# Optimization experiments

Hardware: AMD Instinct MI355X
Metric: run time of the kernel (lower is better)

## Reference

```python
import jax, jax.numpy as jnp
import numpy as np

V = 1_000_000   # number of nodes in graph (embedding table rows)
D_IN = 128      # input feature dim
D_OUT = 384     # output dim (3 * D_OUT//3)
N_UNIQ = 20_000 # unique nodes in batch
K = 32          # neighbors per node (num_walks)
B = 40_000      # batch of node lookups


def setup_inputs() -> dict:
    key = jax.random.key(0)
    ks = jax.random.split(key, 12)
    d3 = D_OUT // 3
    return {
        "unique_nodes": jax.random.randint(ks[0], (N_UNIQ,), 0, V),
        "adj_neighbors": jax.random.randint(ks[1], (N_UNIQ, K), 0, V),
        "dis_neighbors": jax.random.randint(ks[2], (N_UNIQ, K), 0, V),
        "nodes_idx": jax.random.randint(ks[3], (B,), 0, N_UNIQ),
        "feat_table": jax.random.normal(ks[4], (V, D_IN), dtype=jnp.float32),
        # linear weights stored [in, out] (transposed vs torch nn.Linear)
        "W_self": jax.random.uniform(ks[5], (D_IN, d3), minval=-0.1, maxval=0.1, dtype=jnp.float32),
        "W_adj": jax.random.uniform(ks[6], (D_IN, d3), minval=-0.1, maxval=0.1, dtype=jnp.float32),
        "W_dis": jax.random.uniform(ks[7], (D_IN, d3), minval=-0.1, maxval=0.1, dtype=jnp.float32),
        "bias": jnp.zeros((D_OUT,), dtype=jnp.float32),
        "WC_w": jax.random.normal(ks[8], (D_OUT, D_OUT), dtype=jnp.float32) * 0.05,
        "WC_b": jnp.zeros((D_OUT,), dtype=jnp.float32),
    }


def reference(unique_nodes, adj_neighbors, dis_neighbors, nodes_idx,
              feat_table, W_self, W_adj, W_dis, bias, WC_w, WC_b):
    # MeanAggregator: one-hot mask.mm(embed) == mean of gathered neighbor feats
    adj_agg = jnp.mean(feat_table[adj_neighbors], axis=1)   # [N,K,D] -> [N,D]
    dis_agg = jnp.mean(feat_table[dis_neighbors], axis=1)
    self_feats = feat_table[unique_nodes] @ W_self           # [N, D_OUT/3]
    adj_feats = adj_agg @ W_adj
    dis_feats = dis_agg @ W_dis
    # concat + bias, WC linear, leakyReLU(0.2), L2-normalize (eval mode: no dropout)
    feats = jnp.concatenate([self_feats, adj_feats, dis_feats], axis=-1) + bias
    feats = feats @ WC_w + WC_b
    feats = jnp.where(feats >= 0, feats, 0.2 * feats)
    norm = jnp.maximum(jnp.linalg.norm(feats, axis=-1, keepdims=True), 1e-12)
    feats = feats / norm
    return feats[nodes_idx]  # [B, D_OUT]
```

## Files before the change

### kernel.cpp

```cpp
#include <hip/hip_runtime.h>
#include <hip/hip_bf16.h>

#define N_UNIQ 20000
#define K_NBR 32
#define BATCH 40000

typedef unsigned short ushort_t;
typedef __bf16 bfrag __attribute__((ext_vector_type(8)));
typedef float  ffrag __attribute__((ext_vector_type(4)));
typedef unsigned uvec4 __attribute__((ext_vector_type(4)));

__device__ __forceinline__ ushort_t f2bf(float f) {
    unsigned u = __builtin_bit_cast(unsigned, f);
    unsigned r = u + 0x7fffu + ((u >> 16) & 1u);
    return (ushort_t)(r >> 16);
}
__device__ __forceinline__ unsigned pack2(float x, float y) {
    return (unsigned)f2bf(x) | ((unsigned)f2bf(y) << 16);
}

__global__ void pack_agg_kernel(const float* __restrict__ Ws,
                                const float* __restrict__ Wa,
                                const float* __restrict__ Wd,
                                const float* __restrict__ WC,
                                uint4* __restrict__ wp1,
                                uint4* __restrict__ wp2,
                                const int* __restrict__ uniq,
                                const int* __restrict__ adjn,
                                const int* __restrict__ disn,
                                const float* __restrict__ feat,
                                ushort_t* __restrict__ F) {
    if (blockIdx.x < 96) {
        int t = blockIdx.x * blockDim.x + threadIdx.x;
        int l = t & 63, q = l >> 4, m = l & 15;
        ushort_t v[8];
        if (t < 6144) {
            int g   = t >> 11;
            int rem = t & 2047;
            int nt  = rem >> 8;
            int kk  = (rem >> 6) & 3;
            const float* W = (g == 0) ? Ws : ((g == 1) ? Wa : Wd);
#pragma unroll
            for (int j = 0; j < 8; j++)
                v[j] = f2bf(W[(kk * 32 + q * 8 + j) * 128 + nt * 16 + m]);
            uint4 u; __builtin_memcpy(&u, v, 16);
            wp1[t] = u;
        } else {
            int t2 = t - 6144;
            int nt = t2 / 768;
            int kk = (t2 >> 6) % 12;
#pragma unroll
            for (int j = 0; j < 8; j++)
                v[j] = f2bf(WC[(kk * 32 + q * 8 + j) * 384 + nt * 16 + m]);
            uint4 u; __builtin_memcpy(&u, v, 16);
            wp2[t2] = u;
        }
        return;
    }

    int node = ((blockIdx.x - 96) << 2) + (threadIdx.x >> 6);
    node = __builtin_amdgcn_readfirstlane(node);
    if (node >= N_UNIQ) return;

    const int l   = threadIdx.x & 63;
    const int lm  = l & 31;
    const bool isdis = (l >= 32);

    const int* __restrict__ na = adjn + node * K_NBR;
    const int* __restrict__ nd = disn + node * K_NBR;
    const float4* __restrict__ feat4 = (const float4*)feat;

    float ax = 0.f, ay = 0.f, az = 0.f, aw = 0.f;
#pragma unroll
    for (int i = 0; i < K_NBR; i++) {
        int ra = na[i];
        int rd = nd[i];
        int r  = isdis ? rd : ra;
        int idx = r * 32 + lm;
        float4 v = feat4[idx];
        ax += v.x; ay += v.y; az += v.z; aw += v.w;
    }

    const float inv = 1.0f / 32.0f;
    ushort_t* row = F + (size_t)node * 384;

    uint2 mpk;
    mpk.x = pack2(ax * inv, ay * inv);
    mpk.y = pack2(az * inv, aw * inv);
    *(uint2*)(row + 128 + (isdis ? 128 : 0) + lm * 4) = mpk;

    if (!isdis) {
        int rs = uniq[node];
        float4 sv = feat4[rs * 32 + lm];
        uint2 spk;
        spk.x = pack2(sv.x, sv.y);
        spk.y = pack2(sv.z, sv.w);
        *(uint2*)(row + lm * 4) = spk;
    }
}

__global__ void gemm1_kernel(ushort_t* __restrict__ F,
                             const uint4* __restrict__ wp1,
                             const float* __restrict__ bias) {
    int wv = blockIdx.x * 4 + (threadIdx.x >> 6);
    if (wv >= N_UNIQ / 16) return;
    int l = threadIdx.x & 63, q = l >> 4, m = l & 15;
    int m0 = wv * 16;

    uint4 a[12];
    const ushort_t* xrow = F + (size_t)(m0 + m) * 384;
#pragma unroll
    for (int kk = 0; kk < 12; kk++)
        a[kk] = *(const uint4*)(xrow + kk * 32 + q * 8);

    ushort_t outv[24][4];
#pragma unroll
    for (int nt = 0; nt < 24; nt++) {
        int g = nt >> 3;
        ffrag acc = {0.f, 0.f, 0.f, 0.f};
        const uint4* wp = wp1 + (size_t)nt * 4 * 64;
#pragma unroll
        for (int kk = 0; kk < 4; kk++) {
            bfrag bf = __builtin_bit_cast(bfrag, wp[kk * 64 + l]);
            bfrag af = __builtin_bit_cast(bfrag, a[g * 4 + kk]);
            acc = __builtin_amdgcn_mfma_f32_16x16x32_bf16(af, bf, acc, 0, 0, 0);
        }
        float bv = bias[nt * 16 + m];
#pragma unroll
        for (int r = 0; r < 4; r++) outv[nt][r] = f2bf(acc[r] + bv);
    }
#pragma unroll
    for (int nt = 0; nt < 24; nt++) {
        int col = nt * 16 + m;
#pragma unroll
        for (int r = 0; r < 4; r++)
            F[(size_t)(m0 + q * 4 + r) * 384 + col] = outv[nt][r];
    }
}

__global__ void gemm2_kernel(const ushort_t* __restrict__ F,
                             const uint4* __restrict__ wp2,
                             const float* __restrict__ wcb,
                             float* __restrict__ G) {
    int wv = blockIdx.x * 4 + (threadIdx.x >> 6);
    if (wv >= N_UNIQ / 16) return;
    int l = threadIdx.x & 63, q = l >> 4, m = l & 15;
    int m0 = wv * 16;

    uint4 a[12];
    const ushort_t* xrow = F + (size_t)(m0 + m) * 384;
#pragma unroll
    for (int kk = 0; kk < 12; kk++)
        a[kk] = *(const uint4*)(xrow + kk * 32 + q * 8);

    float vals[24][4];
    float ss[4] = {0.f, 0.f, 0.f, 0.f};
#pragma unroll
    for (int nt = 0; nt < 24; nt++) {
        ffrag acc = {0.f, 0.f, 0.f, 0.f};
        const uint4* wp = wp2 + (size_t)nt * 12 * 64;
#pragma unroll
        for (int kk = 0; kk < 12; kk++) {
            bfrag bf = __builtin_bit_cast(bfrag, wp[kk * 64 + l]);
            bfrag af = __builtin_bit_cast(bfrag, a[kk]);
            acc = __builtin_amdgcn_mfma_f32_16x16x32_bf16(af, bf, acc, 0, 0, 0);
        }
        float bv = wcb[nt * 16 + m];
#pragma unroll
        for (int r = 0; r < 4; r++) {
            float v = acc[r] + bv;
            v = (v >= 0.f) ? v : 0.2f * v;
            vals[nt][r] = v;
            ss[r] += v * v;
        }
    }
#pragma unroll
    for (int r = 0; r < 4; r++) {
        float s = ss[r];
        s += __shfl_xor(s, 1);
        s += __shfl_xor(s, 2);
        s += __shfl_xor(s, 4);
        s += __shfl_xor(s, 8);
        float nrm = fmaxf(sqrtf(s), 1e-12f);
        ss[r] = 1.0f / nrm;
    }
#pragma unroll
    for (int nt = 0; nt < 24; nt++) {
        int col = nt * 16 + m;
#pragma unroll
        for (int r = 0; r < 4; r++)
            G[(size_t)(m0 + q * 4 + r) * 384 + col] = vals[nt][r] * ss[r];
    }
}

__global__ void gather_kernel(const int* __restrict__ nidx,
                              const uvec4* __restrict__ G4,
                              uvec4* __restrict__ out4) {
    int t = blockIdx.x * blockDim.x + threadIdx.x;
    if (t >= BATCH * 96) return;
    int b = t / 96, c = t - b * 96;
    int row = nidx[b];
    uvec4 v = G4[(size_t)row * 96 + c];
    __builtin_nontemporal_store(v, &out4[(size_t)b * 96 + c]);
}

extern "C" void kernel_launch(void* const* d_in, const int* in_sizes, int n_in,
                              void* d_out, int out_size, void* d_ws, size_t ws_size,
                              hipStream_t stream) {
    const int*   uniq = (const int*)d_in[0];
    const int*   adjn = (const int*)d_in[1];
    const int*   disn = (const int*)d_in[2];
    const int*   nidx = (const int*)d_in[3];
    const float* feat = (const float*)d_in[4];
    const float* Ws   = (const float*)d_in[5];
    const float* Wa   = (const float*)d_in[6];
    const float* Wd   = (const float*)d_in[7];
    const float* bias = (const float*)d_in[8];
    const float* WC   = (const float*)d_in[9];
    const float* wcb  = (const float*)d_in[10];

    ushort_t* F   = (ushort_t*)d_ws;
    float*    G   = (float*)((char*)d_ws + 15360000);
    uint4*    wp1 = (uint4*)((char*)d_ws + 46080000);
    uint4*    wp2 = (uint4*)((char*)d_ws + 46178304);

    pack_agg_kernel<<<96 + N_UNIQ / 4, 256, 0, stream>>>(
        Ws, Wa, Wd, WC, wp1, wp2, uniq, adjn, disn, feat, F);
    gemm1_kernel<<<(N_UNIQ / 16 + 3) / 4, 256, 0, stream>>>(F, wp1, bias);
    gemm2_kernel<<<(N_UNIQ / 16 + 3) / 4, 256, 0, stream>>>(F, wp2, wcb, G);
    gather_kernel<<<BATCH * 96 / 256, 256, 0, stream>>>(nidx, (const uvec4*)G, (uvec4*)d_out);
}
```

Before: 813.3 us.

## Split GEMM output columns across four waves per 16-row tile

Both GEMM kernels now give each block a single 16-row tile and split the 24 output column tiles across its four waves (6 each), instead of one wave computing all 24. Gemm2 combines per-wave partial sums of squares through shared memory for the L2 norm, and gemm1 adds a block barrier before writing in place into F. The goal is four times more blocks and lower per-wave register pressure, giving better occupancy and latency hiding. The cost is that each A tile is loaded four times, plus extra synchronization.

```diff
diff --git a/kernel.cpp b/kernel.cpp
--- a/kernel.cpp
+++ b/kernel.cpp
@@ -102,10 +102,10 @@
 __global__ void gemm1_kernel(ushort_t* __restrict__ F,
                              const uint4* __restrict__ wp1,
                              const float* __restrict__ bias) {
-    int wv = blockIdx.x * 4 + (threadIdx.x >> 6);
-    if (wv >= N_UNIQ / 16) return;
+    int grp = blockIdx.x;
+    int w   = threadIdx.x >> 6;
     int l = threadIdx.x & 63, q = l >> 4, m = l & 15;
-    int m0 = wv * 16;
+    int m0 = grp * 16;
 
     uint4 a[12];
     const ushort_t* xrow = F + (size_t)(m0 + m) * 384;
@@ -113,10 +113,13 @@
     for (int kk = 0; kk < 12; kk++)
         a[kk] = *(const uint4*)(xrow + kk * 32 + q * 8);
 
-    ushort_t outv[24][4];
-#pragma unroll
-    for (int nt = 0; nt < 24; nt++) {
-        int g = nt >> 3;
+    ushort_t outv[6][4];
+    int nts[6];
+#pragma unroll
+    for (int n = 0; n < 6; n++) {
+        const int g = n >> 1;
+        int nt = g * 8 + w * 2 + (n & 1);
+        nts[n] = nt;
         ffrag acc = {0.f, 0.f, 0.f, 0.f};
         const uint4* wp = wp1 + (size_t)nt * 4 * 64;
 #pragma unroll
@@ -127,14 +130,15 @@
         }
         float bv = bias[nt * 16 + m];
 #pragma unroll
-        for (int r = 0; r < 4; r++) outv[nt][r] = f2bf(acc[r] + bv);
-    }
-#pragma unroll
-    for (int nt = 0; nt < 24; nt++) {
-        int col = nt * 16 + m;
+        for (int r = 0; r < 4; r++) outv[n][r] = f2bf(acc[r] + bv);
+    }
+    __syncthreads();
+#pragma unroll
+    for (int n = 0; n < 6; n++) {
+        int col = nts[n] * 16 + m;
 #pragma unroll
         for (int r = 0; r < 4; r++)
-            F[(size_t)(m0 + q * 4 + r) * 384 + col] = outv[nt][r];
+            F[(size_t)(m0 + q * 4 + r) * 384 + col] = outv[n][r];
     }
 }
 
@@ -142,10 +146,12 @@
                              const uint4* __restrict__ wp2,
                              const float* __restrict__ wcb,
                              float* __restrict__ G) {
-    int wv = blockIdx.x * 4 + (threadIdx.x >> 6);
-    if (wv >= N_UNIQ / 16) return;
+    __shared__ float ssred[4][16];
+    int grp = blockIdx.x;
+    int w   = threadIdx.x >> 6;
+    int nt0 = w * 6;
     int l = threadIdx.x & 63, q = l >> 4, m = l & 15;
-    int m0 = wv * 16;
+    int m0 = grp * 16;
 
     uint4 a[12];
     const ushort_t* xrow = F + (size_t)(m0 + m) * 384;
@@ -153,10 +159,11 @@
     for (int kk = 0; kk < 12; kk++)
         a[kk] = *(const uint4*)(xrow + kk * 32 + q * 8);
 
-    float vals[24][4];
+    float vals[6][4];
     float ss[4] = {0.f, 0.f, 0.f, 0.f};
 #pragma unroll
-    for (int nt = 0; nt < 24; nt++) {
+    for (int n = 0; n < 6; n++) {
+        int nt = nt0 + n;
         ffrag acc = {0.f, 0.f, 0.f, 0.f};
         const uint4* wp = wp2 + (size_t)nt * 12 * 64;
 #pragma unroll
@@ -170,7 +177,7 @@
         for (int r = 0; r < 4; r++) {
             float v = acc[r] + bv;
             v = (v >= 0.f) ? v : 0.2f * v;
-            vals[nt][r] = v;
+            vals[n][r] = v;
             ss[r] += v * v;
         }
     }
@@ -181,15 +188,27 @@
         s += __shfl_xor(s, 2);
         s += __shfl_xor(s, 4);
         s += __shfl_xor(s, 8);
-        float nrm = fmaxf(sqrtf(s), 1e-12f);
-        ss[r] = 1.0f / nrm;
-    }
-#pragma unroll
-    for (int nt = 0; nt < 24; nt++) {
-        int col = nt * 16 + m;
+        ss[r] = s;
+    }
+    if (m == 0) {
+#pragma unroll
+        for (int r = 0; r < 4; r++) ssred[w][q * 4 + r] = ss[r];
+    }
+    __syncthreads();
+
+    float invn[4];
+#pragma unroll
+    for (int r = 0; r < 4; r++) {
+        int row = q * 4 + r;
+        float tot = ssred[0][row] + ssred[1][row] + ssred[2][row] + ssred[3][row];
+        invn[r] = 1.0f / fmaxf(sqrtf(tot), 1e-12f);
+    }
+#pragma unroll
+    for (int n = 0; n < 6; n++) {
+        int col = (nt0 + n) * 16 + m;
 #pragma unroll
         for (int r = 0; r < 4; r++)
-            G[(size_t)(m0 + q * 4 + r) * 384 + col] = vals[nt][r] * ss[r];
+            G[(size_t)(m0 + q * 4 + r) * 384 + col] = vals[n][r] * invn[r];
     }
 }
 
@@ -226,7 +245,7 @@
 
     pack_agg_kernel<<<96 + N_UNIQ / 4, 256, 0, stream>>>(
         Ws, Wa, Wd, WC, wp1, wp2, uniq, adjn, disn, feat, F);
-    gemm1_kernel<<<(N_UNIQ / 16 + 3) / 4, 256, 0, stream>>>(F, wp1, bias);
-    gemm2_kernel<<<(N_UNIQ / 16 + 3) / 4, 256, 0, stream>>>(F, wp2, wcb, G);
+    gemm1_kernel<<<N_UNIQ / 16, 256, 0, stream>>>(F, wp1, bias);
+    gemm2_kernel<<<N_UNIQ / 16, 256, 0, stream>>>(F, wp2, wcb, G);
     gather_kernel<<<BATCH * 96 / 256, 256, 0, stream>>>(nidx, (const uvec4*)G, (uvec4*)d_out);
 }
```

Result: faster. 744.4 us (-8.5%).
